# Kernel tuning notes

Hardware: AMD Instinct MI355X
Metric: run time of the kernel (lower is better)

The kernel has to match this reference:

```python
import jax, jax.numpy as jnp
import numpy as np

DIM = 1024
B, L = 4, 4096


def setup_inputs() -> dict:
    key = jax.random.key(0)
    ks = jax.random.split(key, 6)
    s = 1.0 / np.sqrt(DIM)
    x = jax.random.normal(ks[0], (B, L, DIM), dtype=jnp.float32)
    Wk = jax.random.uniform(ks[1], (DIM, DIM), jnp.float32, -s, s)
    bk = jax.random.uniform(ks[2], (DIM,), jnp.float32, -s, s)
    Wv = jax.random.uniform(ks[3], (DIM, DIM), jnp.float32, -s, s)
    bv = jax.random.uniform(ks[4], (DIM,), jnp.float32, -s, s)
    ln_g = jnp.ones((DIM,), jnp.float32)
    ln_b = jnp.zeros((DIM,), jnp.float32)
    Wo = jax.random.uniform(ks[5], (DIM, DIM), jnp.float32, -s, s)
    bo = jnp.zeros((DIM,), jnp.float32)
    return {"x": x, "Wk": Wk, "bk": bk, "Wv": Wv, "bv": bv,
            "ln_g": ln_g, "ln_b": ln_b, "Wo": Wo, "bo": bo}


def reference(x, Wk, bk, Wv, bv, ln_g, ln_b, Wo, bo):
    B_, L_, D = x.shape
    # key/value projections (torch Linear: x @ W.T + b)
    keys = x @ Wk.T + bk
    keys = keys / jnp.maximum(jnp.linalg.norm(keys, axis=-1, keepdims=True), 1e-12)
    values = x @ Wv.T + bv
    # circular convolution via FFT: bind keys with values
    Kf = jnp.fft.rfft(keys, axis=-1)
    Vf = jnp.fft.rfft(values, axis=-1)
    bound = jnp.fft.irfft(Kf * Vf, n=D, axis=-1)
    # cumulative holographic memory over sequence
    memory = jnp.cumsum(bound, axis=1)
    # circular correlation (unbind): conj of key spectrum
    Mf = jnp.fft.rfft(memory, axis=-1)
    retrieved = jnp.fft.irfft(Mf * jnp.conj(Kf), n=D, axis=-1)
    # position-dependent normalization: sqrt(1..L)
    norm = jnp.sqrt(jnp.arange(1, L_ + 1, dtype=x.dtype)).reshape(1, L_, 1)
    r = retrieved / norm
    # LayerNorm (eps=1e-5) + output Linear
    mu = jnp.mean(r, axis=-1, keepdims=True)
    var = jnp.var(r, axis=-1, keepdims=True)
    r_ln = (r - mu) * jax.lax.rsqrt(var + 1e-5) * ln_g + ln_b
    return x + (r_ln @ Wo.T + bo)
```

## Files before the change

kernel.cpp:

```cpp
#include <hip/hip_runtime.h>
#include <math.h>

#define B_SZ 4
#define L_SZ 4096
#define D_SZ 1024
#define M_SZ (B_SZ * L_SZ)
#define NBINS 513
#define CCH   (2 * NBINS)
#define TLEN 16
#define NCH  (L_SZ / TLEN)
#define NG   16

typedef short bf16x8 __attribute__((ext_vector_type(8)));
typedef float f32x4  __attribute__((ext_vector_type(4)));
typedef unsigned short us8 __attribute__((ext_vector_type(8)));

#define AS1 __attribute__((address_space(1)))
#define AS3 __attribute__((address_space(3)))

__device__ inline unsigned short f2bf(float f) {
    unsigned int u = __float_as_uint(f);
    u += 0x7fffu + ((u >> 16) & 1u);
    return (unsigned short)(u >> 16);
}

__global__ __launch_bounds__(256) void cast_f32_bf16(
        const float* __restrict__ in, unsigned short* __restrict__ out, int n8) {
    int i = blockIdx.x * 256 + threadIdx.x;
    if (i >= n8) return;
    const float4* p = (const float4*)in + 2 * (size_t)i;
    float4 a = p[0], b = p[1];
    us8 o;
    o[0] = f2bf(a.x); o[1] = f2bf(a.y); o[2] = f2bf(a.z); o[3] = f2bf(a.w);
    o[4] = f2bf(b.x); o[5] = f2bf(b.y); o[6] = f2bf(b.z); o[7] = f2bf(b.w);
    *(us8*)(out + (size_t)i * 8) = o;
}

__global__ __launch_bounds__(256) void cast_w3(
        const float* __restrict__ Wk, const float* __restrict__ Wv,
        const float* __restrict__ Wo,
        unsigned short* __restrict__ WB, unsigned short* __restrict__ Wob, int n8) {
    int i = blockIdx.x * 256 + threadIdx.x;
    if (i >= n8) return;
    const int which = blockIdx.y;
    const float* src = (which == 0) ? Wk : (which == 1) ? Wv : Wo;
    unsigned short* dst = (which == 0) ? WB : (which == 1) ? (WB + D_SZ * D_SZ) : Wob;
    const float4* p = (const float4*)src + 2 * (size_t)i;
    float4 a = p[0], b = p[1];
    us8 o;
    o[0] = f2bf(a.x); o[1] = f2bf(a.y); o[2] = f2bf(a.z); o[3] = f2bf(a.w);
    o[4] = f2bf(b.x); o[5] = f2bf(b.y); o[6] = f2bf(b.z); o[7] = f2bf(b.w);
    *(us8*)(dst + (size_t)i * 8) = o;
}

template<int CNT>
__global__ __launch_bounds__(512, 4) void gemm_mfma(
        const unsigned short* __restrict__ A, const unsigned short* __restrict__ W,
        const float* __restrict__ bias0, const float* __restrict__ bias1,
        const float* __restrict__ resid,
        float* __restrict__ C0, float* __restrict__ C1, int M, int K) {
    __shared__ unsigned short Abuf[3][256 * 32];
    __shared__ unsigned short Bbuf[3][128 * 32];
    const int id   = blockIdx.x;
    const int bx   = (id >> 3) % CNT;
    const int by   = (id & 7) + 8 * (id / (8 * CNT));
    const int tid  = threadIdx.x;
    const int lane = tid & 63;
    const int wid  = tid >> 6;
    const int wr   = wid >> 2;
    const int wc   = wid & 3;
    const int bm   = by * 256;
    const int bn   = bx * 128;

    const int sl = tid >> 3;
    const int sq = (tid & 7) ^ (sl & 7);
    const int srow = 2 * sl + (sq >> 2);
    const int skof = (sq & 3) * 8;
    const unsigned short* Abase = A + (size_t)(bm + srow) * K + skof;
    const unsigned short* Wbase = W + (size_t)(bn + srow) * K + skof;
    const int dstoff = tid * 16;

    auto stage3 = [&](int slot, int kk) {
        __builtin_amdgcn_global_load_lds((const AS1 unsigned int*)(Abase + kk),
            (AS3 unsigned int*)((char*)&Abuf[slot][0] + dstoff), 16, 0, 0);
        __builtin_amdgcn_global_load_lds((const AS1 unsigned int*)(Abase + (size_t)128 * K + kk),
            (AS3 unsigned int*)((char*)&Abuf[slot][128 * 32] + dstoff), 16, 0, 0);
        __builtin_amdgcn_global_load_lds((const AS1 unsigned int*)(Wbase + kk),
            (AS3 unsigned int*)((char*)&Bbuf[slot][0] + dstoff), 16, 0, 0);
    };

    const int fr = lane & 15;
    const int kq = lane >> 4;
    const int rslot = (((((fr & 1) << 2) + kq) ^ ((fr >> 1) & 7)) << 4);
    const int aoff0 = wr * 8192 + (fr >> 1) * 128 + rslot;
    const int boff0 = wc * 2048 + (fr >> 1) * 128 + rslot;

    f32x4 acc[8][2] = {};

    const int nt = K >> 5;
    stage3(0, 0);
    stage3(1, 32);
    asm volatile("s_waitcnt vmcnt(3)" ::: "memory");
    __builtin_amdgcn_s_barrier();
    asm volatile("" ::: "memory");

    int slot = 0, slot2 = 2;
    for (int cur = 0; cur < nt; ++cur) {
        bf16x8 a[8], b[2];
        const char* Ab = (const char*)&Abuf[slot][0];
        const char* Bb = (const char*)&Bbuf[slot][0];
        #pragma unroll
        for (int nf = 0; nf < 2; nf++)
            b[nf] = *(const bf16x8*)(Bb + boff0 + nf * 1024);
        #pragma unroll
        for (int mf = 0; mf < 8; mf++)
            a[mf] = *(const bf16x8*)(Ab + aoff0 + mf * 1024);
        if (cur + 2 < nt) stage3(slot2, (cur + 2) << 5);
        __builtin_amdgcn_s_setprio(1);
        #pragma unroll
        for (int mf = 0; mf < 8; mf++)
            #pragma unroll
            for (int nf = 0; nf < 2; nf++)
                acc[mf][nf] = __builtin_amdgcn_mfma_f32_16x16x32_bf16(
                                  a[mf], b[nf], acc[mf][nf], 0, 0, 0);
        __builtin_amdgcn_s_setprio(0);
        if (cur + 2 < nt) { asm volatile("s_waitcnt vmcnt(3)" ::: "memory"); }
        else              { asm volatile("s_waitcnt vmcnt(0)" ::: "memory"); }
        __builtin_amdgcn_s_barrier();
        asm volatile("" ::: "memory");
        slot  = (slot  == 2) ? 0 : slot  + 1;
        slot2 = (slot2 == 2) ? 0 : slot2 + 1;
    }

    const int col0 = lane & 15;
    const int quad = lane >> 4;
    #pragma unroll
    for (int nf = 0; nf < 2; nf++) {
        const int ng = bn + wc * 32 + nf * 16 + col0;
        const int half = ng >> 10;
        const int n = ng & 1023;
        float* __restrict__ Cp = half ? C1 : C0;
        const float bv = half ? bias1[n] : bias0[n];
        #pragma unroll
        for (int mf = 0; mf < 8; mf++) {
            #pragma unroll
            for (int r = 0; r < 4; r++) {
                const int m = bm + wr * 128 + mf * 16 + quad * 4 + r;
                float v = acc[mf][nf][r] + bv;
                size_t off = (size_t)m * 1024 + n;
                if (resid) v += resid[off];
                Cp[off] = v;
            }
        }
    }
}

#define SWZ(a) ((a) ^ (((a) >> 4) & 15))

struct cplx { float r, i; };
__device__ inline cplx cmul(cplx a, cplx b) {
    return {a.r * b.r - a.i * b.i, a.r * b.i + a.i * b.r};
}

__device__ inline void r4bfly(cplx v[4], float s) {
    cplx t0 {v[0].r + v[2].r, v[0].i + v[2].i};
    cplx t1 {v[0].r - v[2].r, v[0].i - v[2].i};
    cplx t2 {v[1].r + v[3].r, v[1].i + v[3].i};
    cplx t3 {v[1].r - v[3].r, v[1].i - v[3].i};
    cplx j3 {-s * t3.i, s * t3.r};
    v[0] = {t0.r + t2.r, t0.i + t2.i};
    v[2] = {t0.r - t2.r, t0.i - t2.i};
    v[1] = {t1.r + j3.r, t1.i + j3.i};
    v[3] = {t1.r - j3.r, t1.i - j3.i};
}

template<int SIGN>
__device__ inline void fft1024_r(float2* bA, float2* bB, cplx v[4], int tid) {
    const float s = (float)SIGN;
    r4bfly(v, s);
    {
        const int base = tid << 2;
        #pragma unroll
        for (int e = 0; e < 4; e++)
            bA[SWZ(base + e)] = make_float2(v[e].r, v[e].i);
    }
    __syncthreads();
    float2* cur = bA;
    float2* nxt = bB;
    #pragma unroll
    for (int q = 1; q <= 3; q++) {
        const int Ls = 1 << (2 * q);
        #pragma unroll
        for (int k = 0; k < 4; k++) {
            float2 t = cur[SWZ(tid + (k << 8))];
            v[k] = {t.x, t.y};
        }
        const int d = tid & (Ls - 1);
        const float ang = s * 1.57079632679489662f * (float)d / (float)Ls;
        float sn, cs; __sincosf(ang, &sn, &cs);
        cplx w1 {cs, sn};
        cplx w2 = cmul(w1, w1);
        cplx w3 = cmul(w2, w1);
        v[1] = cmul(v[1], w1);
        v[2] = cmul(v[2], w2);
        v[3] = cmul(v[3], w3);
        r4bfly(v, s);
        const int base = ((tid >> (2 * q)) << (2 * q + 2)) + d;
        #pragma unroll
        for (int e = 0; e < 4; e++)
            nxt[SWZ(base + (e << (2 * q)))] = make_float2(v[e].r, v[e].i);
        float2* tmp = cur; cur = nxt; nxt = tmp;
        __syncthreads();
    }
    #pragma unroll
    for (int k = 0; k < 4; k++) {
        float2 t = cur[SWZ(tid + (k << 8))];
        v[k] = {t.x, t.y};
    }
    {
        const float ang = s * 1.57079632679489662f * (float)tid / 256.0f;
        float sn, cs; __sincosf(ang, &sn, &cs);
        cplx w1 {cs, sn};
        cplx w2 = cmul(w1, w1);
        cplx w3 = cmul(w2, w1);
        v[1] = cmul(v[1], w1);
        v[2] = cmul(v[2], w2);
        v[3] = cmul(v[3], w3);
        r4bfly(v, s);
    }
}

__global__ __launch_bounds__(256) void bind_cum_kernel(
        float* __restrict__ KIO, const float* __restrict__ V,
        float* __restrict__ P, float* __restrict__ totals) {
    __shared__ float2 bA[1024], bB[1024];
    __shared__ float red[4];
    const int blk = blockIdx.x;
    const int tid = threadIdx.x;
    const int wv  = tid >> 6;
    const int ln  = tid & 63;
    const size_t tok0 = (size_t)blk * TLEN;

    float r0r = 0.f, r0i = 0.f, r1r = 0.f, r1i = 0.f, r2r = 0.f, r2i = 0.f;

    float kvC[4], vvC[4];
    {
        const float* krow = KIO + tok0 * D_SZ;
        const float* vrow = V   + tok0 * D_SZ;
        #pragma unroll
        for (int k = 0; k < 4; k++) {
            kvC[k] = krow[tid + (k << 8)];
            vvC[k] = vrow[tid + (k << 8)];
        }
    }

    for (int tk = 0; tk < TLEN; ++tk) {
        const size_t token = tok0 + tk;
        float* krow = KIO + token * D_SZ;

        float ss = 0.f;
        #pragma unroll
        for (int k = 0; k < 4; k++) ss += kvC[k] * kvC[k];
        #pragma unroll
        for (int m = 1; m < 64; m <<= 1) ss += __shfl_xor(ss, m, 64);
        if (ln == 0) red[wv] = ss;
        __syncthreads();
        const float scale = 1.0f /
            fmaxf(sqrtf(red[0] + red[1] + red[2] + red[3]), 1e-12f);

        cplx z[4];
        #pragma unroll
        for (int k = 0; k < 4; k++) z[k] = {kvC[k] * scale, vvC[k]};

        if (tk + 1 < TLEN) {
            const float* krowN = KIO + (token + 1) * D_SZ;
            const float* vrowN = V   + (token + 1) * D_SZ;
            #pragma unroll
            for (int k = 0; k < 4; k++) {
                kvC[k] = krowN[tid + (k << 8)];
                vvC[k] = vrowN[tid + (k << 8)];
            }
        }

        fft1024_r<-1>(bA, bB, z, tid);

        #pragma unroll
        for (int e = 0; e < 4; e++)
            bA[SWZ(tid + (e << 8))] = make_float2(z[e].r, z[e].i);
        __syncthreads();

        float2* Po = (float2*)(P + token * CCH);
        auto procbin = [&](int bin, float& rr, float& ri) {
            float2 Zb = bA[SWZ(bin)];
            float2 Zm = bA[SWZ((1024 - bin) & 1023)];
            float ar = 0.5f * (Zb.x + Zm.x);
            float ai = 0.5f * (Zb.y - Zm.y);
            float br = 0.5f * (Zb.y + Zm.y);
            float bi = 0.5f * (Zm.x - Zb.x);
            rr += ar * br - ai * bi;
            ri += ar * bi + ai * br;
            Po[bin] = make_float2(rr, ri);
            if (bin == 0)        krow[0] = ar;
            else if (bin == 512) krow[1] = ar;
            else { krow[2 * bin] = ar; krow[2 * bin + 1] = ai; }
        };
        procbin(tid,       r0r, r0i);
        procbin(tid + 256, r1r, r1i);
        if (tid == 0) procbin(512, r2r, r2i);
    }

    float* trow = totals + (size_t)blk * CCH;
    trow[2 * tid]             = r0r;  trow[2 * tid + 1]         = r0i;
    trow[2 * (tid + 256)]     = r1r;  trow[2 * (tid + 256) + 1] = r1i;
    if (tid == 0) { trow[1024] = r2r; trow[1025] = r2i; }
}

__global__ __launch_bounds__(256) void scan_s1(
        float* __restrict__ totals, float* __restrict__ gt) {
    const int c = blockIdx.x * 256 + threadIdx.x;
    if (c >= CCH) return;
    const int g = blockIdx.y;
    const int b = blockIdx.z;
    float run = 0.f;
    #pragma unroll
    for (int i = 0; i < 16; i++) {
        size_t idx = ((size_t)(b * NCH + g * 16 + i)) * CCH + c;
        float v = totals[idx];
        totals[idx] = run;
        run += v;
    }
    gt[((size_t)(b * NG + g)) * CCH + c] = run;
}

__global__ __launch_bounds__(256) void scan_s2(float* __restrict__ gt) {
    const int c = blockIdx.x * 256 + threadIdx.x;
    if (c >= CCH) return;
    const int b = blockIdx.y;
    float run = 0.f;
    #pragma unroll
    for (int g = 0; g < NG; g++) {
        size_t idx = ((size_t)(b * NG + g)) * CCH + c;
        float v = gt[idx];
        gt[idx] = run;
        run += v;
    }
}

__global__ __launch_bounds__(256) void unbind2_ln_kernel(
        const float* __restrict__ P, const float* __restrict__ totals,
        const float* __restrict__ gt, const float* __restrict__ KF,
        const float* __restrict__ ln_g, const float* __restrict__ ln_b,
        unsigned short* __restrict__ RLNb) {
    __shared__ float2 bA[1024], bB[1024];
    __shared__ float red[16];
    const int pair = blockIdx.x;
    const int tid  = threadIdx.x;
    const int wv   = tid >> 6;
    const int ln   = tid & 63;
    const size_t ta = (size_t)pair * 2, tb = ta + 1;
    const int bidx = (int)(ta >> 12);
    const int t_a  = (int)(ta & (L_SZ - 1));
    const int chunk = t_a >> 4;

    const float2* Sa2  = (const float2*)(P + ta * CCH);
    const float2* Sb2  = (const float2*)(P + tb * CCH);
    const float*  Ka   = KF + ta * D_SZ;
    const float*  Kb   = KF + tb * D_SZ;
    const float2* off2 = (const float2*)(totals + (size_t)(bidx * NCH + chunk) * CCH);
    const float2* gof2 = (const float2*)(gt + (size_t)(bidx * NG + (chunk >> 4)) * CCH);

    auto zc = [&](int bin, const float2* S2, const float* kf, float2 og) {
        float kr, ki;
        if (bin == 0)        { kr = kf[0]; ki = 0.f; }
        else if (bin == 512) { kr = kf[1]; ki = 0.f; }
        else { float2 k2 = *(const float2*)(kf + 2 * bin); kr = k2.x; ki = k2.y; }
        float2 s2 = S2[bin];
        float sr = s2.x + og.x, si = s2.y + og.y;
        return make_float2(sr * kr + si * ki, si * kr - sr * ki);
    };
    auto fill = [&](int bin) {
        float2 o = off2[bin], g = gof2[bin];
        float2 og = make_float2(o.x + g.x, o.y + g.y);
        float2 Za = zc(bin, Sa2, Ka, og);
        float2 Zb = zc(bin, Sb2, Kb, og);
        bA[SWZ(bin)] = make_float2(Za.x - Zb.y, Za.y + Zb.x);
        if (bin != 0 && bin != 512)
            bA[SWZ(1024 - bin)] = make_float2(Za.x + Zb.y, Zb.x - Za.y);
    };
    fill(tid);
    fill(tid + 256);
    if (tid == 0) fill(512);
    __syncthreads();

    cplx z[4];
    #pragma unroll
    for (int k = 0; k < 4; k++) {
        float2 c = bA[SWZ(tid + (k << 8))];
        z[k] = {c.x, c.y};
    }
    __syncthreads();
    fft1024_r<1>(bA, bB, z, tid);

    const float sa = (1.0f / 1024.0f) * rsqrtf((float)(t_a + 1));
    const float sb = (1.0f / 1024.0f) * rsqrtf((float)(t_a + 2));
    float ra[4], rb[4];
    float s1a = 0.f, s2a = 0.f, s1b = 0.f, s2b = 0.f;
    #pragma unroll
    for (int e = 0; e < 4; e++) {
        ra[e] = z[e].r * sa;
        rb[e] = z[e].i * sb;
        s1a += ra[e]; s2a += ra[e] * ra[e];
        s1b += rb[e]; s2b += rb[e] * rb[e];
    }
    #pragma unroll
    for (int m = 1; m < 64; m <<= 1) {
        s1a += __shfl_xor(s1a, m, 64);
        s2a += __shfl_xor(s2a, m, 64);
        s1b += __shfl_xor(s1b, m, 64);
        s2b += __shfl_xor(s2b, m, 64);
    }
    if (ln == 0) {
        red[wv] = s1a; red[4 + wv] = s2a; red[8 + wv] = s1b; red[12 + wv] = s2b;
    }
    __syncthreads();
    const float S1a = red[0] + red[1] + red[2] + red[3];
    const float S2a = red[4] + red[5] + red[6] + red[7];
    const float S1b = red[8] + red[9] + red[10] + red[11];
    const float S2b = red[12] + red[13] + red[14] + red[15];
    const float mua = S1a * (1.0f / 1024.0f);
    const float vara = S2a * (1.0f / 1024.0f) - mua * mua;
    const float rsa = rsqrtf(vara + 1e-5f);
    const float mub = S1b * (1.0f / 1024.0f);
    const float varb = S2b * (1.0f / 1024.0f) - mub * mub;
    const float rsb = rsqrtf(varb + 1e-5f);

    unsigned short* outA = RLNb + ta * D_SZ;
    unsigned short* outB = RLNb + tb * D_SZ;
    #pragma unroll
    for (int e = 0; e < 4; e++) {
        const int d = tid + (e << 8);
        const float g = ln_g[d], be = ln_b[d];
        outA[d] = f2bf((ra[e] - mua) * rsa * g + be);
        outB[d] = f2bf((rb[e] - mub) * rsb * g + be);
    }
}

extern "C" void kernel_launch(void* const* d_in, const int* in_sizes, int n_in,
                              void* d_out, int out_size, void* d_ws, size_t ws_size,
                              hipStream_t stream) {
    (void)in_sizes; (void)n_in; (void)out_size; (void)ws_size;
    const float* x    = (const float*)d_in[0];
    const float* Wk   = (const float*)d_in[1];
    const float* bk   = (const float*)d_in[2];
    const float* Wv   = (const float*)d_in[3];
    const float* bv   = (const float*)d_in[4];
    const float* ln_g = (const float*)d_in[5];
    const float* ln_b = (const float*)d_in[6];
    const float* Wo   = (const float*)d_in[7];
    const float* bo   = (const float*)d_in[8];
    float* out = (float*)d_out;

    char* w = (char*)d_ws;
    float* Kraw   = (float*)w;  w += (size_t)M_SZ * D_SZ * 4;
    float* V      = (float*)w;  w += (size_t)M_SZ * D_SZ * 4;
    float* P      = (float*)w;  w += (size_t)M_SZ * CCH * 4;
    float* totals = (float*)w;  w += (size_t)B_SZ * NCH * CCH * 4;
    float* gt     = (float*)w;  w += (size_t)B_SZ * NG * CCH * 4;
    unsigned short* xb  = (unsigned short*)w;  w += (size_t)M_SZ * D_SZ * 2;
    unsigned short* WB  = (unsigned short*)w;  w += (size_t)2 * D_SZ * D_SZ * 2;
    unsigned short* Wob = (unsigned short*)w;  w += (size_t)D_SZ * D_SZ * 2;
    unsigned short* RLNb = (unsigned short*)V;

    const int n8x = M_SZ * D_SZ / 8;
    const int n8w = D_SZ * D_SZ / 8;
    cast_f32_bf16<<<n8x / 256, 256, 0, stream>>>(x, xb, n8x);
    dim3 wgrid(n8w / 256, 3);
    cast_w3<<<wgrid, 256, 0, stream>>>(Wk, Wv, Wo, WB, Wob, n8w);

    gemm_mfma<16><<<(M_SZ / 256) * 16, 512, 0, stream>>>(
        xb, WB, bk, bv, nullptr, Kraw, V, M_SZ, D_SZ);

    bind_cum_kernel<<<M_SZ / TLEN, 256, 0, stream>>>(Kraw, V, P, totals);

    dim3 g1((CCH + 255) / 256, NG, B_SZ);
    scan_s1<<<g1, 256, 0, stream>>>(totals, gt);
    dim3 g2((CCH + 255) / 256, B_SZ);
    scan_s2<<<g2, 256, 0, stream>>>(gt);

    unbind2_ln_kernel<<<M_SZ / 2, 256, 0, stream>>>(
        P, totals, gt, Kraw, ln_g, ln_b, RLNb);

    gemm_mfma<8><<<(M_SZ / 256) * 8, 512, 0, stream>>>(
        RLNb, Wob, bo, bo, x, out, out, M_SZ, D_SZ);
}
```

Before: 417.4 us.

## Halve scan chunk length, precompute FFT twiddles, batch unbind over eight tokens

The chunk length for the cumulative scan drops from 16 to 8 tokens and the group count doubles, so bind_cum runs twice as many blocks, each with a shorter serial loop. FFT twiddle sincos values are now computed once per block instead of on every FFT. The unbind kernel handles four token pairs per block, loading the chunk offsets and LayerNorm gamma/beta once into shared memory and registers. The totals and gt buffers now alias the dead bf16 x workspace. In exchange, the totals array doubles in size, and unbind has fewer blocks, each with a serial loop over pairs.

```diff
diff --git a/kernel.cpp b/kernel.cpp
--- a/kernel.cpp
+++ b/kernel.cpp
@@ -7,9 +7,9 @@
 #define M_SZ (B_SZ * L_SZ)
 #define NBINS 513
 #define CCH   (2 * NBINS)
-#define TLEN 16
+#define TLEN 8
 #define NCH  (L_SZ / TLEN)
-#define NG   16
+#define NG   32
 
 typedef short bf16x8 __attribute__((ext_vector_type(8)));
 typedef float f32x4  __attribute__((ext_vector_type(4)));
@@ -175,7 +175,23 @@
 }
 
 template<int SIGN>
-__device__ inline void fft1024_r(float2* bA, float2* bB, cplx v[4], int tid) {
+__device__ inline void make_w1(cplx w1s[4], int tid) {
+    const float s = (float)SIGN;
+    #pragma unroll
+    for (int q = 1; q <= 3; q++) {
+        const int Ls = 1 << (2 * q);
+        const float ang = s * 1.57079632679489662f * (float)(tid & (Ls - 1)) / (float)Ls;
+        float sn, cs; __sincosf(ang, &sn, &cs);
+        w1s[q - 1] = {cs, sn};
+    }
+    float sn, cs;
+    __sincosf(s * 1.57079632679489662f * (float)tid / 256.0f, &sn, &cs);
+    w1s[3] = {cs, sn};
+}
+
+template<int SIGN>
+__device__ inline void fft1024_tw(float2* bA, float2* bB, cplx v[4], int tid,
+                                  const cplx w1s[4]) {
     const float s = (float)SIGN;
     r4bfly(v, s);
     {
@@ -196,9 +212,7 @@
             v[k] = {t.x, t.y};
         }
         const int d = tid & (Ls - 1);
-        const float ang = s * 1.57079632679489662f * (float)d / (float)Ls;
-        float sn, cs; __sincosf(ang, &sn, &cs);
-        cplx w1 {cs, sn};
+        cplx w1 = w1s[q - 1];
         cplx w2 = cmul(w1, w1);
         cplx w3 = cmul(w2, w1);
         v[1] = cmul(v[1], w1);
@@ -218,9 +232,7 @@
         v[k] = {t.x, t.y};
     }
     {
-        const float ang = s * 1.57079632679489662f * (float)tid / 256.0f;
-        float sn, cs; __sincosf(ang, &sn, &cs);
-        cplx w1 {cs, sn};
+        cplx w1 = w1s[3];
         cplx w2 = cmul(w1, w1);
         cplx w3 = cmul(w2, w1);
         v[1] = cmul(v[1], w1);
@@ -241,6 +253,9 @@
     const int ln  = tid & 63;
     const size_t tok0 = (size_t)blk * TLEN;
 
+    cplx w1s[4];
+    make_w1<-1>(w1s, tid);
+
     float r0r = 0.f, r0i = 0.f, r1r = 0.f, r1i = 0.f, r2r = 0.f, r2i = 0.f;
 
     float kvC[4], vvC[4];
@@ -282,7 +297,7 @@
             }
         }
 
-        fft1024_r<-1>(bA, bB, z, tid);
+        fft1024_tw<-1>(bA, bB, z, tid, w1s);
 
         #pragma unroll
         for (int e = 0; e < 4; e++)
@@ -346,102 +361,126 @@
     }
 }
 
-__global__ __launch_bounds__(256) void unbind2_ln_kernel(
+__global__ __launch_bounds__(256) void unbind4_ln_kernel(
         const float* __restrict__ P, const float* __restrict__ totals,
         const float* __restrict__ gt, const float* __restrict__ KF,
         const float* __restrict__ ln_g, const float* __restrict__ ln_b,
         unsigned short* __restrict__ RLNb) {
     __shared__ float2 bA[1024], bB[1024];
+    __shared__ float2 offsh[NBINS];
     __shared__ float red[16];
-    const int pair = blockIdx.x;
-    const int tid  = threadIdx.x;
-    const int wv   = tid >> 6;
-    const int ln   = tid & 63;
-    const size_t ta = (size_t)pair * 2, tb = ta + 1;
-    const int bidx = (int)(ta >> 12);
-    const int t_a  = (int)(ta & (L_SZ - 1));
-    const int chunk = t_a >> 4;
-
-    const float2* Sa2  = (const float2*)(P + ta * CCH);
-    const float2* Sb2  = (const float2*)(P + tb * CCH);
-    const float*  Ka   = KF + ta * D_SZ;
-    const float*  Kb   = KF + tb * D_SZ;
-    const float2* off2 = (const float2*)(totals + (size_t)(bidx * NCH + chunk) * CCH);
-    const float2* gof2 = (const float2*)(gt + (size_t)(bidx * NG + (chunk >> 4)) * CCH);
-
-    auto zc = [&](int bin, const float2* S2, const float* kf, float2 og) {
-        float kr, ki;
-        if (bin == 0)        { kr = kf[0]; ki = 0.f; }
-        else if (bin == 512) { kr = kf[1]; ki = 0.f; }
-        else { float2 k2 = *(const float2*)(kf + 2 * bin); kr = k2.x; ki = k2.y; }
-        float2 s2 = S2[bin];
-        float sr = s2.x + og.x, si = s2.y + og.y;
-        return make_float2(sr * kr + si * ki, si * kr - sr * ki);
-    };
-    auto fill = [&](int bin) {
-        float2 o = off2[bin], g = gof2[bin];
-        float2 og = make_float2(o.x + g.x, o.y + g.y);
-        float2 Za = zc(bin, Sa2, Ka, og);
-        float2 Zb = zc(bin, Sb2, Kb, og);
-        bA[SWZ(bin)] = make_float2(Za.x - Zb.y, Za.y + Zb.x);
-        if (bin != 0 && bin != 512)
-            bA[SWZ(1024 - bin)] = make_float2(Za.x + Zb.y, Zb.x - Za.y);
-    };
-    fill(tid);
-    fill(tid + 256);
-    if (tid == 0) fill(512);
+    const int blk = blockIdx.x;
+    const int tid = threadIdx.x;
+    const int wv  = tid >> 6;
+    const int ln  = tid & 63;
+    const size_t tok0 = (size_t)blk * TLEN;
+    const int bidx  = (int)(tok0 >> 12);
+    const int t0    = (int)(tok0 & (L_SZ - 1));
+    const int chunk = t0 >> 3;
+
+    {
+        const float2* off2 = (const float2*)(totals + (size_t)(bidx * NCH + chunk) * CCH);
+        const float2* gof2 = (const float2*)(gt + (size_t)(bidx * NG + (chunk >> 4)) * CCH);
+        auto ldo = [&](int bin) {
+            float2 o = off2[bin], g = gof2[bin];
+            offsh[bin] = make_float2(o.x + g.x, o.y + g.y);
+        };
+        ldo(tid); ldo(tid + 256);
+        if (tid == 0) ldo(512);
+    }
+
+    cplx w1s[4];
+    make_w1<1>(w1s, tid);
+
+    float gv[4], bev[4];
+    #pragma unroll
+    for (int e = 0; e < 4; e++) {
+        gv[e]  = ln_g[tid + (e << 8)];
+        bev[e] = ln_b[tid + (e << 8)];
+    }
     __syncthreads();
 
-    cplx z[4];
-    #pragma unroll
-    for (int k = 0; k < 4; k++) {
-        float2 c = bA[SWZ(tid + (k << 8))];
-        z[k] = {c.x, c.y};
-    }
-    __syncthreads();
-    fft1024_r<1>(bA, bB, z, tid);
-
-    const float sa = (1.0f / 1024.0f) * rsqrtf((float)(t_a + 1));
-    const float sb = (1.0f / 1024.0f) * rsqrtf((float)(t_a + 2));
-    float ra[4], rb[4];
-    float s1a = 0.f, s2a = 0.f, s1b = 0.f, s2b = 0.f;
-    #pragma unroll
-    for (int e = 0; e < 4; e++) {
-        ra[e] = z[e].r * sa;
-        rb[e] = z[e].i * sb;
-        s1a += ra[e]; s2a += ra[e] * ra[e];
-        s1b += rb[e]; s2b += rb[e] * rb[e];
-    }
-    #pragma unroll
-    for (int m = 1; m < 64; m <<= 1) {
-        s1a += __shfl_xor(s1a, m, 64);
-        s2a += __shfl_xor(s2a, m, 64);
-        s1b += __shfl_xor(s1b, m, 64);
-        s2b += __shfl_xor(s2b, m, 64);
-    }
-    if (ln == 0) {
-        red[wv] = s1a; red[4 + wv] = s2a; red[8 + wv] = s1b; red[12 + wv] = s2b;
-    }
-    __syncthreads();
-    const float S1a = red[0] + red[1] + red[2] + red[3];
-    const float S2a = red[4] + red[5] + red[6] + red[7];
-    const float S1b = red[8] + red[9] + red[10] + red[11];
-    const float S2b = red[12] + red[13] + red[14] + red[15];
-    const float mua = S1a * (1.0f / 1024.0f);
-    const float vara = S2a * (1.0f / 1024.0f) - mua * mua;
-    const float rsa = rsqrtf(vara + 1e-5f);
-    const float mub = S1b * (1.0f / 1024.0f);
-    const float varb = S2b * (1.0f / 1024.0f) - mub * mub;
-    const float rsb = rsqrtf(varb + 1e-5f);
-
-    unsigned short* outA = RLNb + ta * D_SZ;
-    unsigned short* outB = RLNb + tb * D_SZ;
-    #pragma unroll
-    for (int e = 0; e < 4; e++) {
-        const int d = tid + (e << 8);
-        const float g = ln_g[d], be = ln_b[d];
-        outA[d] = f2bf((ra[e] - mua) * rsa * g + be);
-        outB[d] = f2bf((rb[e] - mub) * rsb * g + be);
+    for (int p = 0; p < 4; ++p) {
+        const size_t ta = tok0 + 2 * p, tb = ta + 1;
+        const float2* Sa2 = (const float2*)(P + ta * CCH);
+        const float2* Sb2 = (const float2*)(P + tb * CCH);
+        const float*  Ka  = KF + ta * D_SZ;
+        const float*  Kb  = KF + tb * D_SZ;
+
+        auto zc = [&](int bin, const float2* S2, const float* kf, float2 og) {
+            float kr, ki;
+            if (bin == 0)        { kr = kf[0]; ki = 0.f; }
+            else if (bin == 512) { kr = kf[1]; ki = 0.f; }
+            else { float2 k2 = *(const float2*)(kf + 2 * bin); kr = k2.x; ki = k2.y; }
+            float2 s2 = S2[bin];
+            float sr = s2.x + og.x, si = s2.y + og.y;
+            return make_float2(sr * kr + si * ki, si * kr - sr * ki);
+        };
+        auto fill = [&](int bin) {
+            float2 og = offsh[bin];
+            float2 Za = zc(bin, Sa2, Ka, og);
+            float2 Zb = zc(bin, Sb2, Kb, og);
+            bA[SWZ(bin)] = make_float2(Za.x - Zb.y, Za.y + Zb.x);
+            if (bin != 0 && bin != 512)
+                bA[SWZ(1024 - bin)] = make_float2(Za.x + Zb.y, Zb.x - Za.y);
+        };
+        fill(tid);
+        fill(tid + 256);
+        if (tid == 0) fill(512);
+        __syncthreads();
+
+        cplx z[4];
+        #pragma unroll
+        for (int k = 0; k < 4; k++) {
+            float2 c = bA[SWZ(tid + (k << 8))];
+            z[k] = {c.x, c.y};
+        }
+        __syncthreads();
+        fft1024_tw<1>(bA, bB, z, tid, w1s);
+
+        const int t_a = t0 + 2 * p;
+        const float sa = (1.0f / 1024.0f) * rsqrtf((float)(t_a + 1));
+        const float sb = (1.0f / 1024.0f) * rsqrtf((float)(t_a + 2));
+        float ra[4], rb[4];
+        float s1a = 0.f, s2a = 0.f, s1b = 0.f, s2b = 0.f;
+        #pragma unroll
+        for (int e = 0; e < 4; e++) {
+            ra[e] = z[e].r * sa;
+            rb[e] = z[e].i * sb;
+            s1a += ra[e]; s2a += ra[e] * ra[e];
+            s1b += rb[e]; s2b += rb[e] * rb[e];
+        }
+        #pragma unroll
+        for (int m = 1; m < 64; m <<= 1) {
+            s1a += __shfl_xor(s1a, m, 64);
+            s2a += __shfl_xor(s2a, m, 64);
+            s1b += __shfl_xor(s1b, m, 64);
+            s2b += __shfl_xor(s2b, m, 64);
+        }
+        if (ln == 0) {
+            red[wv] = s1a; red[4 + wv] = s2a; red[8 + wv] = s1b; red[12 + wv] = s2b;
+        }
+        __syncthreads();
+        const float S1a = red[0] + red[1] + red[2] + red[3];
+        const float S2a = red[4] + red[5] + red[6] + red[7];
+        const float S1b = red[8] + red[9] + red[10] + red[11];
+        const float S2b = red[12] + red[13] + red[14] + red[15];
+        const float mua = S1a * (1.0f / 1024.0f);
+        const float vara = S2a * (1.0f / 1024.0f) - mua * mua;
+        const float rsa = rsqrtf(vara + 1e-5f);
+        const float mub = S1b * (1.0f / 1024.0f);
+        const float varb = S2b * (1.0f / 1024.0f) - mub * mub;
+        const float rsb = rsqrtf(varb + 1e-5f);
+
+        unsigned short* outA = RLNb + ta * D_SZ;
+        unsigned short* outB = RLNb + tb * D_SZ;
+        #pragma unroll
+        for (int e = 0; e < 4; e++) {
+            const int d = tid + (e << 8);
+            outA[d] = f2bf((ra[e] - mua) * rsa * gv[e] + bev[e]);
+            outB[d] = f2bf((rb[e] - mub) * rsb * gv[e] + bev[e]);
+        }
+        __syncthreads();
     }
 }
 
@@ -464,12 +503,12 @@
     float* Kraw   = (float*)w;  w += (size_t)M_SZ * D_SZ * 4;
     float* V      = (float*)w;  w += (size_t)M_SZ * D_SZ * 4;
     float* P      = (float*)w;  w += (size_t)M_SZ * CCH * 4;
-    float* totals = (float*)w;  w += (size_t)B_SZ * NCH * CCH * 4;
-    float* gt     = (float*)w;  w += (size_t)B_SZ * NG * CCH * 4;
     unsigned short* xb  = (unsigned short*)w;  w += (size_t)M_SZ * D_SZ * 2;
     unsigned short* WB  = (unsigned short*)w;  w += (size_t)2 * D_SZ * D_SZ * 2;
     unsigned short* Wob = (unsigned short*)w;  w += (size_t)D_SZ * D_SZ * 2;
     unsigned short* RLNb = (unsigned short*)V;
+    float* totals = (float*)xb;
+    float* gt     = (float*)xb + (size_t)B_SZ * NCH * CCH;
 
     const int n8x = M_SZ * D_SZ / 8;
     const int n8w = D_SZ * D_SZ / 8;
@@ -487,7 +526,7 @@
     dim3 g2((CCH + 255) / 256, B_SZ);
     scan_s2<<<g2, 256, 0, stream>>>(gt);
 
-    unbind2_ln_kernel<<<M_SZ / 2, 256, 0, stream>>>(
+    unbind4_ln_kernel<<<M_SZ / TLEN, 256, 0, stream>>>(
         P, totals, gt, Kraw, ln_g, ln_b, RLNb);
 
     gemm_mfma<8><<<(M_SZ / 256) * 8, 512, 0, stream>>>(
```

New measurement: 391.2 us. -6.3%, faster.
